# Performance work log

Hardware: AMD Instinct MI355X
Metric: run time of the kernel (lower is better)

The kernel has to match this reference:

```python
import jax, jax.numpy as jnp
import numpy as np

F, H, E, D, B = 1024, 256, 64, 64, 4096
N = F + H


def setup_inputs() -> dict:
    key = jax.random.key(0)
    k = jax.random.split(key, 7)
    values = jax.random.normal(k[0], (B, F), dtype=jnp.float32)
    # GlorotNormal-ish init for embeddings and dense layers
    feat_emb = jax.random.normal(k[1], (F, E), dtype=jnp.float32) * (2.0 / (F + E)) ** 0.5
    hidden_emb = jax.random.normal(k[2], (H, E), dtype=jnp.float32) * (2.0 / (H + E)) ** 0.5
    w_kernel = jax.random.normal(k[3], (2 * E, D), dtype=jnp.float32) * (2.0 / (2 * E + D)) ** 0.5
    w_bias = jnp.zeros((D,), dtype=jnp.float32)
    u_kernel = jax.random.normal(k[4], (D,), dtype=jnp.float32) * (2.0 / (D + 1)) ** 0.5
    # sparse ancestor mask; every node is its own ancestor -> diagonal True
    mask = jax.random.bernoulli(k[5], 0.02, (F, N))
    mask = mask.at[jnp.arange(F), jnp.arange(F)].set(True)
    return {
        "values": values,
        "feat_emb": feat_emb,
        "hidden_emb": hidden_emb,
        "w_kernel": w_kernel,
        "w_bias": w_bias,
        "u_kernel": u_kernel,
        "mask": mask,
    }


def reference(values, feat_emb, hidden_emb, w_kernel, w_bias, u_kernel, mask):
    # full embedding table: [N, E]
    full = jnp.concatenate([feat_emb, hidden_emb], axis=0)
    # Dense(w) applied to concat([e_i, f_j]) == e_i @ Wa + f_j @ Wb + b
    Wa, Wb = w_kernel[:E], w_kernel[E:]
    feat_proj = feat_emb @ Wa            # [F, D]
    full_proj = full @ Wb                # [N, D]
    h = jnp.tanh(feat_proj[:, None, :] + full_proj[None, :, :] + w_bias)  # [F, N, D]
    score = jnp.einsum("fnd,d->fn", h, u_kernel)  # [F, N]
    # masked exp / normalize (faithful to tf.where(mask, exp(score), 0) / sum)
    escore = jnp.where(mask, jnp.exp(score), 0.0)
    attn = escore / jnp.sum(escore, axis=1, keepdims=True)  # [F, N]
    context = attn @ full                # [F, E]
    return values @ context              # [B, E]
```

## Files before the change

kernel.cpp:

```cpp
#include <hip/hip_runtime.h>
#include <stdint.h>

#define F 1024
#define H 256
#define E 64
#define D 64
#define B 4096
#define NN 1280

typedef __attribute__((ext_vector_type(8))) short bf16x8;
typedef __attribute__((ext_vector_type(4))) float f32x4;
typedef unsigned long long ull;

__device__ inline uint16_t f2bf_rne(float x) {
    union { float f; uint32_t u; } v; v.f = x;
    uint32_t u = v.u + 0x7fffu + ((v.u >> 16) & 1u);
    return (uint16_t)(u >> 16);
}
__device__ inline float bf2f(uint16_t h) {
    union { uint32_t u; float f; } v; v.u = ((uint32_t)h) << 16;
    return v.f;
}
__device__ inline void split8(float4 a, float4 b, bf16x8& hi, bf16x8& lo) {
    float v[8] = {a.x, a.y, a.z, a.w, b.x, b.y, b.z, b.w};
#pragma unroll
    for (int j = 0; j < 8; ++j) {
        uint16_t h = f2bf_rne(v[j]);
        hi[j] = (short)h;
        lo[j] = (short)f2bf_rne(v[j] - bf2f(h));
    }
}

__global__ __launch_bounds__(256)
void attn_kernel(const float* __restrict__ feat_emb,
                 const float* __restrict__ hidden_emb,
                 const float* __restrict__ w_kernel,
                 const float* __restrict__ w_bias,
                 const float* __restrict__ u_kernel,
                 const void*  __restrict__ mask,
                 uint16_t* __restrict__ ctxB_hi,
                 uint16_t* __restrict__ ctxB_lo) {
    __shared__ float s_full[64][64];
    __shared__ unsigned short s_idxw[4][32];
    __shared__ unsigned short s_idxb[64];
    __shared__ int   s_cnt4[4];
    __shared__ float s_feat[64], s_fp[64];
    __shared__ float s_sc[64], s_es[64];
    __shared__ float s_cacc[4][64];
    __shared__ int   s_mode;

    int tid = threadIdx.x;
    int w = tid >> 6, lane = tid & 63;
    int f = blockIdx.x;

    if (w == 0) {
        s_feat[lane] = feat_emb[(size_t)f * E + lane];
        long e = (long)lane * (NN + 1);
        bool okb = ((const uint8_t*)mask)[e] == 1;
        bool oki = ((const int*)mask)[e] == 1;
        bool okf = ((const float*)mask)[e] == 1.0f;
        ull bb = __ballot(okb), bi = __ballot(oki), bf = __ballot(okf);
        if (lane == 0) {
            int m = 0;
            if (bb == ~0ull) m = 0;
            else if (bi == ~0ull) m = 1;
            else if (bf == ~0ull) m = 2;
            s_mode = m;
        }
    }
    __syncthreads();
    int mode = s_mode;

    {
        const uint8_t* mb = (const uint8_t*)mask;
        const int*     mi = (const int*)mask;
        const float*   mf = (const float*)mask;
        bool mv[5];
        long base = (long)f * NN + w * 320;
#pragma unroll
        for (int c = 0; c < 5; ++c) {
            long midx = base + c * 64 + lane;
            if (mode == 0)      mv[c] = (mb[midx] != 0);
            else if (mode == 1) mv[c] = (mi[midx] != 0);
            else                mv[c] = (mf[midx] != 0.f);
        }
        ull below = lane ? (~0ull >> (64 - lane)) : 0ull;
        int cw = 0;
#pragma unroll
        for (int c = 0; c < 5; ++c) {
            ull bal = __ballot(mv[c]);
            if (mv[c]) {
                int pos = cw + __popcll(bal & below);
                if (pos < 32) s_idxw[w][pos] = (unsigned short)(w * 320 + c * 64 + lane);
            }
            cw += __popcll(bal);
        }
        cw = min(cw, 32);
        if (lane == 0) s_cnt4[w] = cw;
    }
    __syncthreads();
    int c0 = s_cnt4[0], c1 = s_cnt4[1], c2 = s_cnt4[2], c3 = s_cnt4[3];
    int cnt = min(c0 + c1 + c2 + c3, 64);
    {
        int offw = (w > 0 ? c0 : 0) + (w > 1 ? c1 : 0) + (w > 2 ? c2 : 0);
        int cw = s_cnt4[w];
        if (lane < cw) {
            int p = offw + lane;
            if (p < 64) s_idxb[p] = s_idxw[w][lane];
        }
    }
    __syncthreads();

    int i_e = w * 16 + (lane & 15);
    bool valid = i_e < cnt;
    int n = valid ? (int)s_idxb[i_e] : 0;
    int e0 = (lane >> 4) * 8;
    const float* rowp = (n < F) ? (feat_emb + (size_t)n * E)
                                : (hidden_emb + (size_t)(n - F) * E);
    float4 z4 = {0.f, 0.f, 0.f, 0.f};
    float4 r00 = valid ? *(const float4*)(rowp + e0)          : z4;
    float4 r01 = valid ? *(const float4*)(rowp + e0 + 4)      : z4;
    float4 r10 = valid ? *(const float4*)(rowp + 32 + e0)     : z4;
    float4 r11 = valid ? *(const float4*)(rowp + 32 + e0 + 4) : z4;
    *(float4*)&s_full[i_e][e0]          = r00;
    *(float4*)&s_full[i_e][e0 + 4]      = r01;
    *(float4*)&s_full[i_e][32 + e0]     = r10;
    *(float4*)&s_full[i_e][32 + e0 + 4] = r11;
    bf16x8 ahi[2], alo[2];
    split8(r00, r01, ahi[0], alo[0]);
    split8(r10, r11, ahi[1], alo[1]);

    float uv[4], bvv[4];
#pragma unroll
    for (int nt = 0; nt < 4; ++nt) {
        int d = nt * 16 + (lane & 15);
        uv[nt]  = u_kernel[d];
        bvv[nt] = w_bias[d];
    }

    if (w == 3) {
        float a0 = 0.f, a1 = 0.f, a2 = 0.f, a3 = 0.f;
#pragma unroll
        for (int e = 0; e < 64; e += 4) {
            a0 = fmaf(s_feat[e + 0], w_kernel[(size_t)(e + 0) * 64 + lane], a0);
            a1 = fmaf(s_feat[e + 1], w_kernel[(size_t)(e + 1) * 64 + lane], a1);
            a2 = fmaf(s_feat[e + 2], w_kernel[(size_t)(e + 2) * 64 + lane], a2);
            a3 = fmaf(s_feat[e + 3], w_kernel[(size_t)(e + 3) * 64 + lane], a3);
        }
        s_fp[lane] = (a0 + a1) + (a2 + a3);
    }

    int tile_n = min(16, cnt - w * 16);
    bool do_mfma = tile_n > 0;
    f32x4 acc[4];
#pragma unroll
    for (int nt = 0; nt < 4; ++nt) acc[nt] = (f32x4){0.f, 0.f, 0.f, 0.f};
    if (do_mfma) {
#pragma unroll
        for (int nt = 0; nt < 4; ++nt) {
            int d = nt * 16 + (lane & 15);
            bf16x8 bh0, bl0, bh1, bl1;
#pragma unroll
            for (int j = 0; j < 8; ++j) {
                float v0 = w_kernel[(size_t)(64 + e0 + j) * 64 + d];
                float v1 = w_kernel[(size_t)(64 + 32 + e0 + j) * 64 + d];
                uint16_t h0 = f2bf_rne(v0); bh0[j] = (short)h0; bl0[j] = (short)f2bf_rne(v0 - bf2f(h0));
                uint16_t h1 = f2bf_rne(v1); bh1[j] = (short)h1; bl1[j] = (short)f2bf_rne(v1 - bf2f(h1));
            }
            acc[nt] = __builtin_amdgcn_mfma_f32_16x16x32_bf16(ahi[0], bh0, acc[nt], 0, 0, 0);
            acc[nt] = __builtin_amdgcn_mfma_f32_16x16x32_bf16(ahi[0], bl0, acc[nt], 0, 0, 0);
            acc[nt] = __builtin_amdgcn_mfma_f32_16x16x32_bf16(alo[0], bh0, acc[nt], 0, 0, 0);
            acc[nt] = __builtin_amdgcn_mfma_f32_16x16x32_bf16(ahi[1], bh1, acc[nt], 0, 0, 0);
            acc[nt] = __builtin_amdgcn_mfma_f32_16x16x32_bf16(ahi[1], bl1, acc[nt], 0, 0, 0);
            acc[nt] = __builtin_amdgcn_mfma_f32_16x16x32_bf16(alo[1], bh1, acc[nt], 0, 0, 0);
        }
    }
    __syncthreads();

    const float k2E = 2.885390082f;
    const float kE  = 1.44269504f;
    if (do_mfma) {
        float ts[4] = {0.f, 0.f, 0.f, 0.f};
#pragma unroll
        for (int nt = 0; nt < 4; ++nt) {
            int d = nt * 16 + (lane & 15);
            float fpv = s_fp[d];
#pragma unroll
            for (int r = 0; r < 4; ++r) {
                float x  = acc[nt][r] + fpv + bvv[nt];
                float ax = fminf(fabsf(x), 10.f);
                float ex = exp2f(k2E * ax);
                float th = (ex - 1.f) * __builtin_amdgcn_rcpf(ex + 1.f);
                th = copysignf(th, x);
                ts[r] = fmaf(th, uv[nt], ts[r]);
            }
        }
#pragma unroll
        for (int r = 0; r < 4; ++r) {
            float t = ts[r];
            t += __shfl_xor(t, 1); t += __shfl_xor(t, 2);
            t += __shfl_xor(t, 4); t += __shfl_xor(t, 8);
            if ((lane & 15) == 0) s_sc[w * 16 + (lane >> 4) * 4 + r] = t;
        }
    }
    __syncthreads();

    if (w == 0) {
        float es = (lane < cnt) ? exp2f(kE * s_sc[lane]) : 0.f;
        float s = es;
#pragma unroll
        for (int off = 1; off <= 32; off <<= 1) s += __shfl_xor(s, off);
        s_es[lane] = es / s;
    }
    __syncthreads();

    {
        float cacc = 0.f;
        int lim = min(16, cnt - w * 16);
        for (int k = 0; k < lim; ++k) {
            int i = w * 16 + k;
            cacc = fmaf(s_es[i], s_full[i][lane], cacc);
        }
        s_cacc[w][lane] = cacc;
    }
    __syncthreads();
    if (w == 0) {
        float c = s_cacc[0][lane] + s_cacc[1][lane] + s_cacc[2][lane] + s_cacc[3][lane];
        uint16_t hi = f2bf_rne(c);
        float lof = c - bf2f(hi);
        uint16_t lo = f2bf_rne(lof);
        int ks = f >> 5, kk = f & 31;
        int ch = kk >> 3, j = kk & 7;
        int l2 = ch * 16 + (lane & 15);
        int nt = lane >> 4;
        int off = ((ks * 4 + nt) * 64 + l2) * 8 + j;
        ctxB_hi[off] = hi;
        ctxB_lo[off] = lo;
    }
}

#define OKW 16
__global__ __launch_bounds__(1024, 4)
void out_kernel(const float* __restrict__ values,
                const uint16_t* __restrict__ ctxB_hi,
                const uint16_t* __restrict__ ctxB_lo,
                float* __restrict__ out) {
    __shared__ float red[OKW][16][64];
    int tid = threadIdx.x;
    int w = tid >> 6, l = tid & 63;
    int m0 = blockIdx.x * 16;
    f32x4 acc[4];
#pragma unroll
    for (int nt = 0; nt < 4; ++nt) acc[nt] = (f32x4){0.f, 0.f, 0.f, 0.f};
    int row = m0 + (l & 15);
    int kchunk = (l >> 4) * 8;
#pragma unroll
    for (int s = 0; s < 2; ++s) {
        int ks = w * 2 + s;
        int k0 = ks * 32 + kchunk;
        const float4 va0 = *reinterpret_cast<const float4*>(values + (size_t)row * F + k0);
        const float4 va1 = *reinterpret_cast<const float4*>(values + (size_t)row * F + k0 + 4);
        bf16x8 ahi, alo;
        split8(va0, va1, ahi, alo);
#pragma unroll
        for (int nt = 0; nt < 4; ++nt) {
            int boff = ((ks * 4 + nt) * 64 + l) * 8;
            bf16x8 bhi = *reinterpret_cast<const bf16x8*>(ctxB_hi + boff);
            bf16x8 blo = *reinterpret_cast<const bf16x8*>(ctxB_lo + boff);
            acc[nt] = __builtin_amdgcn_mfma_f32_16x16x32_bf16(ahi, bhi, acc[nt], 0, 0, 0);
            acc[nt] = __builtin_amdgcn_mfma_f32_16x16x32_bf16(ahi, blo, acc[nt], 0, 0, 0);
            acc[nt] = __builtin_amdgcn_mfma_f32_16x16x32_bf16(alo, bhi, acc[nt], 0, 0, 0);
        }
    }
#pragma unroll
    for (int nt = 0; nt < 4; ++nt)
#pragma unroll
        for (int r = 0; r < 4; ++r) {
            int orow = (l >> 4) * 4 + r;
            int ocol = nt * 16 + (l & 15);
            red[w][orow][ocol] = acc[nt][r];
        }
    __syncthreads();
    int orow = tid >> 6, ocol = tid & 63;
    float s2 = 0.f;
#pragma unroll
    for (int ww = 0; ww < OKW; ++ww) s2 += red[ww][orow][ocol];
    out[(size_t)(m0 + orow) * D + ocol] = s2;
}

extern "C" void kernel_launch(void* const* d_in, const int* in_sizes, int n_in,
                              void* d_out, int out_size, void* d_ws, size_t ws_size,
                              hipStream_t stream) {
    const float* values     = (const float*)d_in[0];
    const float* feat_emb   = (const float*)d_in[1];
    const float* hidden_emb = (const float*)d_in[2];
    const float* w_kernel   = (const float*)d_in[3];
    const float* w_bias     = (const float*)d_in[4];
    const float* u_kernel   = (const float*)d_in[5];
    const void*  mask       = (const void*)d_in[6];
    float* out = (float*)d_out;

    uint16_t* ctxB_hi = (uint16_t*)d_ws;
    uint16_t* ctxB_lo = ctxB_hi + 32 * 4 * 64 * 8;

    attn_kernel<<<F, 256, 0, stream>>>(feat_emb, hidden_emb, w_kernel, w_bias,
                                       u_kernel, mask, ctxB_hi, ctxB_lo);
    out_kernel<<<B / 16, 1024, 0, stream>>>(values, ctxB_hi, ctxB_lo, out);
}
```

Before: 31.18 us.

## Precompute feature projection and split Wb fragments in a prep kernel

Adds a prep kernel that computes feat_emb @ Wa for all features, pre-splits Wb into hi/lo bf16 MFMA fragment layout, and detects the mask dtype once. The attention kernel then loads these from workspace instead of redoing the projection and conversion in every block. It also XOR-swizzles the shared s_full layout to reduce LDS bank conflicts. The cost is an extra kernel launch and a global round trip for the precomputed data.

```diff
diff --git a/kernel.cpp b/kernel.cpp
--- a/kernel.cpp
+++ b/kernel.cpp
@@ -32,29 +32,46 @@
 }
 
 __global__ __launch_bounds__(256)
-void attn_kernel(const float* __restrict__ feat_emb,
-                 const float* __restrict__ hidden_emb,
+void prep_kernel(const float* __restrict__ feat_emb,
                  const float* __restrict__ w_kernel,
-                 const float* __restrict__ w_bias,
-                 const float* __restrict__ u_kernel,
                  const void*  __restrict__ mask,
-                 uint16_t* __restrict__ ctxB_hi,
-                 uint16_t* __restrict__ ctxB_lo) {
-    __shared__ float s_full[64][64];
-    __shared__ unsigned short s_idxw[4][32];
-    __shared__ unsigned short s_idxb[64];
-    __shared__ int   s_cnt4[4];
-    __shared__ float s_feat[64], s_fp[64];
-    __shared__ float s_sc[64], s_es[64];
-    __shared__ float s_cacc[4][64];
-    __shared__ int   s_mode;
-
+                 float* __restrict__ fp,
+                 uint16_t* __restrict__ wbB_hi, uint16_t* __restrict__ wbB_lo,
+                 int* __restrict__ flag) {
     int tid = threadIdx.x;
-    int w = tid >> 6, lane = tid & 63;
-    int f = blockIdx.x;
-
-    if (w == 0) {
-        s_feat[lane] = feat_emb[(size_t)f * E + lane];
+    if (blockIdx.x < 256) {
+        int r = blockIdx.x * 4 + (tid >> 6);
+        int d = tid & 63;
+        const float* emb = feat_emb + (size_t)r * E;
+        float a0 = 0.f, a1 = 0.f, a2 = 0.f, a3 = 0.f;
+#pragma unroll
+        for (int e = 0; e < E; e += 4) {
+            a0 = fmaf(emb[e + 0], w_kernel[(size_t)(e + 0) * D + d], a0);
+            a1 = fmaf(emb[e + 1], w_kernel[(size_t)(e + 1) * D + d], a1);
+            a2 = fmaf(emb[e + 2], w_kernel[(size_t)(e + 2) * D + d], a2);
+            a3 = fmaf(emb[e + 3], w_kernel[(size_t)(e + 3) * D + d], a3);
+        }
+        fp[(size_t)r * D + d] = (a0 + a1) + (a2 + a3);
+        return;
+    }
+#pragma unroll
+    for (int s = tid; s < 512; s += 256) {
+        int l = s & 63, nt = (s >> 6) & 3, ks = s >> 8;
+        int d = nt * 16 + (l & 15);
+        int eb = ks * 32 + (l >> 4) * 8;
+        bf16x8 hi, lo;
+#pragma unroll
+        for (int j = 0; j < 8; ++j) {
+            float v = w_kernel[(size_t)(E + eb + j) * D + d];
+            uint16_t h = f2bf_rne(v);
+            hi[j] = (short)h;
+            lo[j] = (short)f2bf_rne(v - bf2f(h));
+        }
+        *(bf16x8*)(wbB_hi + (size_t)s * 8) = hi;
+        *(bf16x8*)(wbB_lo + (size_t)s * 8) = lo;
+    }
+    if (tid < 64) {
+        int lane = tid;
         long e = (long)lane * (NN + 1);
         bool okb = ((const uint8_t*)mask)[e] == 1;
         bool oki = ((const int*)mask)[e] == 1;
@@ -65,11 +82,37 @@
             if (bb == ~0ull) m = 0;
             else if (bi == ~0ull) m = 1;
             else if (bf == ~0ull) m = 2;
-            s_mode = m;
-        }
-    }
-    __syncthreads();
-    int mode = s_mode;
+            *flag = m;
+        }
+    }
+}
+
+__global__ __launch_bounds__(256)
+void attn_kernel(const float* __restrict__ feat_emb,
+                 const float* __restrict__ hidden_emb,
+                 const float* __restrict__ w_bias,
+                 const float* __restrict__ u_kernel,
+                 const void*  __restrict__ mask,
+                 const float* __restrict__ fp,
+                 const uint16_t* __restrict__ wbB_hi,
+                 const uint16_t* __restrict__ wbB_lo,
+                 const int* __restrict__ flag,
+                 uint16_t* __restrict__ ctxB_hi,
+                 uint16_t* __restrict__ ctxB_lo) {
+    __shared__ float s_full[64][64];
+    __shared__ unsigned short s_idxw[4][32];
+    __shared__ unsigned short s_idxb[64];
+    __shared__ int   s_cnt4[4];
+    __shared__ float s_fp[64];
+    __shared__ float s_sc[64], s_es[64];
+    __shared__ float s_cacc[4][64];
+
+    int tid = threadIdx.x;
+    int w = tid >> 6, lane = tid & 63;
+    int f = blockIdx.x;
+    int mode = flag[0];
+
+    if (w == 0) s_fp[lane] = fp[(size_t)f * D + lane];
 
     {
         const uint8_t* mb = (const uint8_t*)mask;
@@ -122,10 +165,11 @@
     float4 r01 = valid ? *(const float4*)(rowp + e0 + 4)      : z4;
     float4 r10 = valid ? *(const float4*)(rowp + 32 + e0)     : z4;
     float4 r11 = valid ? *(const float4*)(rowp + 32 + e0 + 4) : z4;
-    *(float4*)&s_full[i_e][e0]          = r00;
-    *(float4*)&s_full[i_e][e0 + 4]      = r01;
-    *(float4*)&s_full[i_e][32 + e0]     = r10;
-    *(float4*)&s_full[i_e][32 + e0 + 4] = r11;
+    int sw = (i_e & 7) << 3;
+    *(float4*)&s_full[i_e][e0 ^ sw]        = r00;
+    *(float4*)&s_full[i_e][(e0 ^ sw) + 4]  = r01;
+    *(float4*)&s_full[i_e][(32 + e0) ^ sw]       = r10;
+    *(float4*)&s_full[i_e][((32 + e0) ^ sw) + 4] = r11;
     bf16x8 ahi[2], alo[2];
     split8(r00, r01, ahi[0], alo[0]);
     split8(r10, r11, ahi[1], alo[1]);
@@ -138,18 +182,6 @@
         bvv[nt] = w_bias[d];
     }
 
-    if (w == 3) {
-        float a0 = 0.f, a1 = 0.f, a2 = 0.f, a3 = 0.f;
-#pragma unroll
-        for (int e = 0; e < 64; e += 4) {
-            a0 = fmaf(s_feat[e + 0], w_kernel[(size_t)(e + 0) * 64 + lane], a0);
-            a1 = fmaf(s_feat[e + 1], w_kernel[(size_t)(e + 1) * 64 + lane], a1);
-            a2 = fmaf(s_feat[e + 2], w_kernel[(size_t)(e + 2) * 64 + lane], a2);
-            a3 = fmaf(s_feat[e + 3], w_kernel[(size_t)(e + 3) * 64 + lane], a3);
-        }
-        s_fp[lane] = (a0 + a1) + (a2 + a3);
-    }
-
     int tile_n = min(16, cnt - w * 16);
     bool do_mfma = tile_n > 0;
     f32x4 acc[4];
@@ -158,15 +190,12 @@
     if (do_mfma) {
 #pragma unroll
         for (int nt = 0; nt < 4; ++nt) {
-            int d = nt * 16 + (lane & 15);
-            bf16x8 bh0, bl0, bh1, bl1;
-#pragma unroll
-            for (int j = 0; j < 8; ++j) {
-                float v0 = w_kernel[(size_t)(64 + e0 + j) * 64 + d];
-                float v1 = w_kernel[(size_t)(64 + 32 + e0 + j) * 64 + d];
-                uint16_t h0 = f2bf_rne(v0); bh0[j] = (short)h0; bl0[j] = (short)f2bf_rne(v0 - bf2f(h0));
-                uint16_t h1 = f2bf_rne(v1); bh1[j] = (short)h1; bl1[j] = (short)f2bf_rne(v1 - bf2f(h1));
-            }
+            size_t b0 = ((size_t)(0 * 4 + nt) * 64 + lane) * 8;
+            size_t b1 = ((size_t)(1 * 4 + nt) * 64 + lane) * 8;
+            bf16x8 bh0 = *(const bf16x8*)(wbB_hi + b0);
+            bf16x8 bl0 = *(const bf16x8*)(wbB_lo + b0);
+            bf16x8 bh1 = *(const bf16x8*)(wbB_hi + b1);
+            bf16x8 bl1 = *(const bf16x8*)(wbB_lo + b1);
             acc[nt] = __builtin_amdgcn_mfma_f32_16x16x32_bf16(ahi[0], bh0, acc[nt], 0, 0, 0);
             acc[nt] = __builtin_amdgcn_mfma_f32_16x16x32_bf16(ahi[0], bl0, acc[nt], 0, 0, 0);
             acc[nt] = __builtin_amdgcn_mfma_f32_16x16x32_bf16(alo[0], bh0, acc[nt], 0, 0, 0);
@@ -219,7 +248,7 @@
         int lim = min(16, cnt - w * 16);
         for (int k = 0; k < lim; ++k) {
             int i = w * 16 + k;
-            cacc = fmaf(s_es[i], s_full[i][lane], cacc);
+            cacc = fmaf(s_es[i], s_full[i][lane ^ ((i & 7) << 3)], cacc);
         }
         s_cacc[w][lane] = cacc;
     }
@@ -300,10 +329,18 @@
     const void*  mask       = (const void*)d_in[6];
     float* out = (float*)d_out;
 
-    uint16_t* ctxB_hi = (uint16_t*)d_ws;
-    uint16_t* ctxB_lo = ctxB_hi + 32 * 4 * 64 * 8;
-
-    attn_kernel<<<F, 256, 0, stream>>>(feat_emb, hidden_emb, w_kernel, w_bias,
-                                       u_kernel, mask, ctxB_hi, ctxB_lo);
+    int*      wsi     = (int*)d_ws;
+    float*    wsf     = (float*)d_ws;
+    float*    fp      = wsf + 64;
+    uint16_t* wbB_hi  = (uint16_t*)(fp + F * D);
+    uint16_t* wbB_lo  = wbB_hi + 4096;
+    uint16_t* ctxB_hi = wbB_lo + 4096;
+    uint16_t* ctxB_lo = ctxB_hi + 65536;
+
+    prep_kernel<<<257, 256, 0, stream>>>(feat_emb, w_kernel, mask,
+                                         fp, wbB_hi, wbB_lo, wsi);
+    attn_kernel<<<F, 256, 0, stream>>>(feat_emb, hidden_emb, w_bias, u_kernel,
+                                       mask, fp, wbB_hi, wbB_lo, wsi,
+                                       ctxB_hi, ctxB_lo);
     out_kernel<<<B / 16, 1024, 0, stream>>>(values, ctxB_hi, ctxB_lo, out);
 }
```

New measurement: 28.80 us. 1.08x faster.
